# Performance work log

Measured on AMD Instinct MI355X. Metric: run time of the kernel, lower is better.

The kernel has to match this reference:

```python
import jax, jax.numpy as jnp
import numpy as np

# Quantization configuration mirroring the module-level constants in the source
INPUT_BIT, WEIGHT_BIT, OUTPUT_BIT, DAC_BIT, ADC_BIT = 8, 4, 8, 2, 8
N_SLICES = INPUT_BIT // DAC_BIT  # 4 bit-serial DAC slices of 2 bits each


def ste_round(v):
    # straight-through estimator round (fake-quant / LSQ style)
    return v + jax.lax.stop_gradient(jnp.round(v) - v)


def setup_inputs() -> dict:
    key = jax.random.key(0)
    k1, k2, k3 = jax.random.split(key, 3)
    B, IN_F, OUT_F = 32768, 1024, 1024
    x = jax.random.normal(k1, (B, IN_F), jnp.float32)
    weight = jax.random.normal(k2, (OUT_F, IN_F), jnp.float32) * 0.02
    bias = jax.random.normal(k3, (OUT_F,), jnp.float32) * 0.01
    # LSQ step sizes (learned scalars) for input / weight / output fake-quant
    s_x = jnp.float32(4.0 / 255.0)
    s_w = jnp.float32(0.01)
    s_o = jnp.float32(0.05)
    # per-output-column ADC gain (adc_adjust_mode='gain'); noise scales are 0 -> deterministic
    gain = jnp.ones((OUT_F,), jnp.float32)
    return {"x": x, "weight": weight, "bias": bias, "s_x": s_x, "s_w": s_w, "s_o": s_o, "gain": gain}


def reference(x, weight, bias, s_x, s_w, s_o, gain):
    QP_IN = float(2 ** INPUT_BIT - 1)                      # unsigned 8-bit activations
    QN_W, QP_W = float(-2 ** (WEIGHT_BIT - 1)), float(2 ** (WEIGHT_BIT - 1) - 1)  # signed 4-bit weights
    QN_A, QP_A = float(-2 ** (ADC_BIT - 1)), float(2 ** (ADC_BIT - 1) - 1)        # 8-bit ADC
    QN_O, QP_O = float(-2 ** (OUTPUT_BIT - 1)), float(2 ** (OUTPUT_BIT - 1) - 1)  # signed 8-bit output

    # --- input / weight fake quantization (LSQ) ---
    x_int = ste_round(jnp.clip(x / s_x, 0.0, QP_IN))       # [B, in_f] integer codes (float dtype)
    w_int = ste_round(jnp.clip(weight / s_w, QN_W, QP_W))  # [out_f, in_f]

    # ideal integer matmul result (differentiable path)
    ideal = jnp.matmul(x_int, w_int.T) * (s_x * s_w)       # [B, out_f]

    # --- bit-serial DAC slicing + per-slice ADC (hardware emulation, non-diff) ---
    xi = jax.lax.stop_gradient(x_int)
    wi = jax.lax.stop_gradient(w_int)
    g = jax.lax.stop_gradient(gain)                        # [out_f]
    base = float(2 ** DAC_BIT)
    acc = jnp.zeros((x.shape[0], weight.shape[0]), x.dtype)
    for i in range(N_SLICES):  # fixed small loop (4 slices)
        shift = base ** i
        sl = jnp.mod(jnp.floor(xi / shift), base)          # 2-bit slice in {0,1,2,3}
        partial = jnp.matmul(sl, wi.T)                     # analog MAC result [B, out_f]
        adc = jnp.clip(jnp.round(partial * g), QN_A, QP_A) / g  # ADC quant with column gain
        acc = acc + adc * shift
    out_cim = acc * (s_x * s_w)

    # straight-through: forward value = CIM-emulated, gradient = ideal path
    out = ideal + jax.lax.stop_gradient(out_cim - ideal) + bias

    # --- output fake quantization ---
    y = s_o * ste_round(jnp.clip(out / s_o, QN_O, QP_O))
    return y
```

## Files before the change

kernel.cpp:

```cpp
#pragma float_control(precise, on)
#include <hip/hip_runtime.h>
#include <stdint.h>


typedef int   i32x4 __attribute__((ext_vector_type(4)));

#define MDIM   32768
#define KDIM   1024
#define NDIM   1024
#define ABLK   131072

__device__ __forceinline__ void gload16(const void* g, void* l) {
  __builtin_amdgcn_global_load_lds(
      (const __attribute__((address_space(1))) void*)g,
      (__attribute__((address_space(3))) void*)l,
      16, 0, 0);
}

__global__ __launch_bounds__(256) void quant_x_kernel(
    const float* __restrict__ x, const float* __restrict__ s_x_p,
    uint8_t* __restrict__ Aq, uint8_t* __restrict__ rowFlag) {
  const float rcp = 1.0f / s_x_p[0];
  const int tid = blockIdx.x * 256 + threadIdx.x;
  const int m   = tid >> 6;
  const int k16 = tid & 63;
  const float* xp = x + (size_t)m * KDIM + k16 * 16;
  float vv[16];
#pragma unroll
  for (int q = 0; q < 4; ++q) {
    const float4 v = *(const float4*)(xp + q * 4);
    vv[q * 4 + 0] = v.x; vv[q * 4 + 1] = v.y; vv[q * 4 + 2] = v.z; vv[q * 4 + 3] = v.w;
  }
  int c[16];
  bool anyAmb = false;
#pragma unroll
  for (int j = 0; j < 16; ++j) {
    const float t  = vv[j] * rcp;
    const float tc = fminf(fmaxf(t, 0.0f), 255.0f);
    const float kf = rintf(tc);
    c[j] = (int)kf;
    const float d = 0.5f - fabsf(tc - kf);
    anyAmb = anyAmb || (d < 4e-7f * (tc + 1.0f));
  }
  if (anyAmb) rowFlag[m] = 1;
  const int bm  = m >> 5;
  const int wr  = (m >> 4) & 1;
  const int mi  = (m >> 2) & 3;
  const int fr4 = (m & 3) * 4;
  const int kt  = k16 >> 2, fk = k16 & 3;
  uint8_t* base = Aq + (size_t)bm * ABLK + kt * 8192 + ((wr * 4 + mi) << 10)
                  + (fk * 16 + fr4) * 16;
#pragma unroll
  for (int s = 0; s < 4; ++s) {
    uint32_t w[4];
#pragma unroll
    for (int q = 0; q < 4; ++q) {
      w[q] =  (uint32_t)((c[q*4+0] >> (2*s)) & 3)
           | ((uint32_t)((c[q*4+1] >> (2*s)) & 3) << 8)
           | ((uint32_t)((c[q*4+2] >> (2*s)) & 3) << 16)
           | ((uint32_t)((c[q*4+3] >> (2*s)) & 3) << 24);
    }
    *(uint4*)(base + s * 16) = make_uint4(w[0], w[1], w[2], w[3]);
  }
}

__global__ __launch_bounds__(256) void quant_w_kernel(
    const float* __restrict__ wgt, const float* __restrict__ s_w_p,
    uint8_t* __restrict__ Bq, int* __restrict__ colInfo) {
  const float rcp = 1.0f / s_w_p[0];
  const int tid = blockIdx.x * 256 + threadIdx.x;
  const int n   = tid >> 6;
  const int k16 = tid & 63;
  const float* wp = wgt + (size_t)n * KDIM + k16 * 16;
  float vv[16];
#pragma unroll
  for (int q = 0; q < 4; ++q) {
    const float4 v = *(const float4*)(wp + q * 4);
    vv[q * 4 + 0] = v.x; vv[q * 4 + 1] = v.y; vv[q * 4 + 2] = v.z; vv[q * 4 + 3] = v.w;
  }
  uint32_t w[4];
#pragma unroll
  for (int q = 0; q < 4; ++q) w[q] = 0;
#pragma unroll
  for (int j = 0; j < 16; ++j) {
    const float t  = vv[j] * rcp;
    const float tc = fminf(fmaxf(t, -8.0f), 7.0f);
    const float kf = rintf(tc);
    const int   iv = (int)kf;
    const float fr = tc - kf;
    const float d  = 0.5f - fabsf(fr);
    if (d < 4e-7f * (fabsf(tc) + 1.0f)) {
      const int jj = k16 * 16 + j;
      colInfo[n] = (jj << 2) | ((fr > 0.0f) ? 2 : 0) | 1;
    }
    w[j >> 2] |= (uint32_t)((uint8_t)iv) << (8 * (j & 3));
  }
  const int bn  = n >> 7;
  const int rl  = n & 127;
  const int wc  = rl >> 6;
  const int ni  = (rl >> 4) & 3;
  const int fr_ = rl & 15;
  const int kt  = k16 >> 2, fk = k16 & 3;
  uint8_t* dst = Bq + (size_t)bn * ABLK + kt * 8192 + ((wc * 4 + ni) << 10)
                 + (fk * 16 + fr_) * 16;
  *(uint4*)dst = make_uint4(w[0], w[1], w[2], w[3]);
}

struct ChainOut { float kf; float tc; };
__device__ __forceinline__ ChainOut cim_chain(float p0, float p1, float p2, float p3,
                                              float bi, float sxsw, float rcp_so) {
#pragma clang fp contract(off)
  const float a0 = fminf(fmaxf(p0, -128.f), 127.f);
  const float a1 = fminf(fmaxf(p1, -128.f), 127.f);
  const float a2 = fminf(fmaxf(p2, -128.f), 127.f);
  const float a3 = fminf(fmaxf(p3, -128.f), 127.f);
  float acc_i = a0 + a1 * 4.f;
  acc_i = acc_i + a2 * 16.f;
  acc_i = acc_i + a3 * 64.f;
  float idl_i = p0 + p1 * 4.f;
  idl_i = idl_i + p2 * 16.f;
  idl_i = idl_i + p3 * 64.f;
  const float cim  = acc_i * sxsw;
  const float idea = idl_i * sxsw;
  float ov = idea + (cim - idea);
  ov = ov + bi;
  const float t  = ov * rcp_so;
  const float tc = fminf(fmaxf(t, -128.f), 127.f);
  ChainOut r; r.kf = rintf(tc); r.tc = tc; return r;
}

__global__ __launch_bounds__(256) void gemm_cim(
    const uint8_t* __restrict__ Aq, const uint8_t* __restrict__ Bq,
    const float* __restrict__ bias, const float* __restrict__ gain,
    const float* __restrict__ s_x_p, const float* __restrict__ s_w_p,
    const float* __restrict__ s_o_p, const uint8_t* __restrict__ rowFlag,
    const int* __restrict__ colInfo, float* __restrict__ C) {
  __shared__ uint8_t sA[8192];
  __shared__ uint8_t sB[8192];

  const int t    = threadIdx.x;
  const int l    = (blockIdx.x & 7) * 1024 + (blockIdx.x >> 3);
  const int bn   = l & 7;
  const int bm   = l >> 3;
  const int lane = t & 63;
  const int wv   = t >> 6;
  const int wr   = wv >> 1, wc = wv & 1;
  const int fr   = lane & 15, lk = lane >> 4;

  const uint8_t* gA = Aq + (size_t)bm * ABLK;
  const uint8_t* gB = Bq + (size_t)bn * ABLK;

  i32x4 acc[4][4];
#pragma unroll
  for (int i = 0; i < 4; ++i)
#pragma unroll
    for (int j = 0; j < 4; ++j) acc[i][j] = (i32x4){0, 0, 0, 0};

  const int lofs = lane * 16;
  for (int kt = 0; kt < KDIM / 64; ++kt) {
    __syncthreads();
#pragma unroll
    for (int r = 0; r < 2; ++r) {
      const int o = t * 16 + r * 4096;
      gload16(gA + kt * 8192 + o, sA + o);
      gload16(gB + kt * 8192 + o, sB + o);
    }
    __syncthreads();

    i32x4 a[4], b[4];
#pragma unroll
    for (int mi = 0; mi < 4; ++mi)
      a[mi] = *(const i32x4*)(sA + ((wr * 4 + mi) << 10) + lofs);
#pragma unroll
    for (int ni = 0; ni < 4; ++ni)
      b[ni] = *(const i32x4*)(sB + ((wc * 4 + ni) << 10) + lofs);

#pragma unroll
    for (int mi = 0; mi < 4; ++mi)
#pragma unroll
      for (int ni = 0; ni < 4; ++ni)
        acc[mi][ni] = __builtin_amdgcn_mfma_i32_16x16x64_i8(a[mi], b[ni], acc[mi][ni], 0, 0, 0);
  }

  {
#pragma clang fp contract(off)
    const float sxf = s_x_p[0], swf = s_w_p[0], sof = s_o_p[0];
    const float sxsw   = sxf * swf;
    const float rcp_so = 1.0f / sof;
#pragma unroll
    for (int ni = 0; ni < 4; ++ni) {
      const int   col = bn * 128 + wc * 64 + ni * 16 + fr;
      const float g   = gain[col];
      const float bi  = bias[col];
      const int   ci  = colInfo[col];
#pragma unroll
      for (int mi = 0; mi < 4; ++mi) {
        const int rowA = bm * 128 + wr * 64 + mi * 16 + lk * 4;
        const int m    = rowA >> 2;
        const i32x4 pi = acc[mi][ni];
        const float p0 = (float)pi[0], p1 = (float)pi[1];
        const float p2 = (float)pi[2], p3 = (float)pi[3];
        float y;
        if (g == 1.0f) {
          const ChainOut c0 = cim_chain(p0, p1, p2, p3, bi, sxsw, rcp_so);
          bool done = false;
          if (ci & 1) {
            const int   jj  = ci >> 2;
            const float dir = (ci & 2) ? 1.f : -1.f;
            const uint8_t* ab = Aq + (size_t)(m >> 5) * ABLK + (jj >> 6) * 8192
                                + ((((m >> 4) & 1) * 4 + ((m >> 2) & 3)) << 10)
                                + ((((jj >> 4) & 3) * 16 + (m & 3) * 4) * 16) + (jj & 15);
            const float q0 = (float)ab[0];
            const float q1 = (float)ab[16];
            const float q2 = (float)ab[32];
            const float q3 = (float)ab[48];
            const ChainOut c1 = cim_chain(p0 + dir * q0, p1 + dir * q1,
                                          p2 + dir * q2, p3 + dir * q3,
                                          bi, sxsw, rcp_so);
            if (c1.kf != c0.kf) {
              y = sof * (0.5f * (c0.kf + c1.kf));
              done = true;
            }
          }
          if (!done) {
            const float frac = c0.tc - c0.kf;
            const float d    = 0.5f - fabsf(frac);
            const float eps  = rowFlag[m] ? 0.03f : 1e-3f;
            if (d < eps && frac != 0.0f)
              y = sof * (c0.kf + ((frac > 0.0f) ? 0.5f : -0.5f));
            else
              y = sof * c0.kf;
          }
        } else {
          float a0 = fminf(fmaxf(rintf(p0 * g), -128.f), 127.f) / g;
          float a1 = fminf(fmaxf(rintf(p1 * g), -128.f), 127.f) / g;
          float a2 = fminf(fmaxf(rintf(p2 * g), -128.f), 127.f) / g;
          float a3 = fminf(fmaxf(rintf(p3 * g), -128.f), 127.f) / g;
          float acc_i = ((a0 + a1 * 4.f) + a2 * 16.f) + a3 * 64.f;
          float idl_i = ((p0 + p1 * 4.f) + p2 * 16.f) + p3 * 64.f;
          float ov = idl_i * sxsw + (acc_i * sxsw - idl_i * sxsw) + bi;
          float tc = fminf(fmaxf(ov * rcp_so, -128.f), 127.f);
          y = sof * rintf(tc);
        }
        C[(size_t)m * NDIM + col] = y;
      }
    }
  }
}

extern "C" void kernel_launch(void* const* d_in, const int* in_sizes, int n_in,
                              void* d_out, int out_size, void* d_ws, size_t ws_size,
                              hipStream_t stream) {
  const float* x    = (const float*)d_in[0];
  const float* wgt  = (const float*)d_in[1];
  const float* bias = (const float*)d_in[2];
  const float* s_x  = (const float*)d_in[3];
  const float* s_w  = (const float*)d_in[4];
  const float* s_o  = (const float*)d_in[5];
  const float* gain = (const float*)d_in[6];
  float* C = (float*)d_out;

  const size_t aq_bytes = (size_t)1024 * ABLK;
  const size_t bq_bytes = (size_t)8 * ABLK;
  const size_t fl_bytes = MDIM + NDIM * sizeof(int);
  if (ws_size < aq_bytes + bq_bytes + fl_bytes) return;

  uint8_t* Aq      = (uint8_t*)d_ws;
  uint8_t* Bq      = Aq + aq_bytes;
  uint8_t* rowFlag = Bq + bq_bytes;
  int*     colInfo = (int*)(rowFlag + MDIM);

  hipMemsetAsync(rowFlag, 0, fl_bytes, stream);
  quant_x_kernel<<<dim3(8192), dim3(256), 0, stream>>>(x, s_x, Aq, rowFlag);
  quant_w_kernel<<<dim3(256),  dim3(256), 0, stream>>>(wgt, s_w, Bq, colInfo);
  gemm_cim<<<dim3(8192), dim3(256), 0, stream>>>(Aq, Bq, bias, gain, s_x, s_w, s_o,
                                                 rowFlag, colInfo, C);
}
```

Baseline: 285.5 us.

## Double-buffer LDS tiles in CIM GEMM to overlap global loads with MFMA

Splits the LDS staging buffers into two halves and prefetches the next K tile with direct global-to-LDS loads while the current tile is consumed by MFMA instructions. Partial vmcnt waits and raw s_barrier calls replace the two full __syncthreads per iteration. The goal is to hide global memory latency behind the int8 matrix work, at the cost of doubled LDS use (32 KB per block), which may lower occupancy. Correctness relies on the hand-written waitcnt counts and on LDS reads finishing before the buffer is overwritten.

```diff
diff --git a/kernel.cpp b/kernel.cpp
--- a/kernel.cpp
+++ b/kernel.cpp
@@ -135,8 +135,8 @@
     const float* __restrict__ s_x_p, const float* __restrict__ s_w_p,
     const float* __restrict__ s_o_p, const uint8_t* __restrict__ rowFlag,
     const int* __restrict__ colInfo, float* __restrict__ C) {
-  __shared__ uint8_t sA[8192];
-  __shared__ uint8_t sB[8192];
+  __shared__ uint8_t sA[2][8192];
+  __shared__ uint8_t sB[2][8192];
 
   const int t    = threadIdx.x;
   const int l    = (blockIdx.x & 7) * 1024 + (blockIdx.x >> 3);
@@ -157,30 +157,45 @@
     for (int j = 0; j < 4; ++j) acc[i][j] = (i32x4){0, 0, 0, 0};
 
   const int lofs = lane * 16;
-  for (int kt = 0; kt < KDIM / 64; ++kt) {
-    __syncthreads();
-#pragma unroll
-    for (int r = 0; r < 2; ++r) {
-      const int o = t * 16 + r * 4096;
-      gload16(gA + kt * 8192 + o, sA + o);
-      gload16(gB + kt * 8192 + o, sB + o);
-    }
-    __syncthreads();
-
+  const int o0 = t * 16, o1 = t * 16 + 4096;
+
+  auto STAGE = [&](int kt, int bf) {
+    gload16(gA + kt * 8192 + o0, sA[bf] + o0);
+    gload16(gA + kt * 8192 + o1, sA[bf] + o1);
+    gload16(gB + kt * 8192 + o0, sB[bf] + o0);
+    gload16(gB + kt * 8192 + o1, sB[bf] + o1);
+  };
+  auto COMPUTE = [&](int bf) {
     i32x4 a[4], b[4];
 #pragma unroll
     for (int mi = 0; mi < 4; ++mi)
-      a[mi] = *(const i32x4*)(sA + ((wr * 4 + mi) << 10) + lofs);
+      a[mi] = *(const i32x4*)(sA[bf] + ((wr * 4 + mi) << 10) + lofs);
 #pragma unroll
     for (int ni = 0; ni < 4; ++ni)
-      b[ni] = *(const i32x4*)(sB + ((wc * 4 + ni) << 10) + lofs);
-
+      b[ni] = *(const i32x4*)(sB[bf] + ((wc * 4 + ni) << 10) + lofs);
 #pragma unroll
     for (int mi = 0; mi < 4; ++mi)
 #pragma unroll
       for (int ni = 0; ni < 4; ++ni)
         acc[mi][ni] = __builtin_amdgcn_mfma_i32_16x16x64_i8(a[mi], b[ni], acc[mi][ni], 0, 0, 0);
-  }
+  };
+
+  STAGE(0, 0);
+  int cur = 0;
+  for (int kt = 0; kt < 15; ++kt) {
+    STAGE(kt + 1, cur ^ 1);
+    asm volatile("s_waitcnt vmcnt(4)" ::: "memory");
+    __builtin_amdgcn_sched_barrier(0);
+    __builtin_amdgcn_s_barrier();
+    COMPUTE(cur);
+    __builtin_amdgcn_sched_barrier(0);
+    __builtin_amdgcn_s_barrier();
+    cur ^= 1;
+  }
+  asm volatile("s_waitcnt vmcnt(0)" ::: "memory");
+  __builtin_amdgcn_sched_barrier(0);
+  __builtin_amdgcn_s_barrier();
+  COMPUTE(cur);
 
   {
 #pragma clang fp contract(off)
```

Measured after the change: 266.4 us. -6.7%, faster.

## Enlarge GEMM tile to 256x256 with 512 threads and triple-buffered LDS prefetch

Applied to the files above, without the earlier changes.

Doubles the GEMM block tile (256 rows of packed slices by 256 columns) and uses 8 waves per block. The quantized A/B packing is rearranged to match the new tile, and each wave now holds 8x4 accumulators. A three-stage LDS ring buffer issues global-to-LDS loads two k-steps ahead, interleaved with the MFMA bursts under explicit waitcnt, barriers and setprio. The goal is to raise data reuse and hide global load latency. In exchange it uses 96KB of LDS and more accumulator registers, which may limit occupancy, and adds many barriers per k-step.

```diff
diff --git a/kernel.cpp b/kernel.cpp
--- a/kernel.cpp
+++ b/kernel.cpp
@@ -3,12 +3,13 @@
 #include <stdint.h>
 
 
-typedef int   i32x4 __attribute__((ext_vector_type(4)));
+typedef int i32x4 __attribute__((ext_vector_type(4)));
 
 #define MDIM   32768
 #define KDIM   1024
 #define NDIM   1024
-#define ABLK   131072
+#define TBLK   262144
+#define KTS    16384
 
 __device__ __forceinline__ void gload16(const void* g, void* l) {
   __builtin_amdgcn_global_load_lds(
@@ -43,13 +44,11 @@
     anyAmb = anyAmb || (d < 4e-7f * (tc + 1.0f));
   }
   if (anyAmb) rowFlag[m] = 1;
-  const int bm  = m >> 5;
-  const int wr  = (m >> 4) & 1;
-  const int mi  = (m >> 2) & 3;
+  const int bm  = m >> 6;
+  const int g   = (m >> 2) & 15;
   const int fr4 = (m & 3) * 4;
-  const int kt  = k16 >> 2, fk = k16 & 3;
-  uint8_t* base = Aq + (size_t)bm * ABLK + kt * 8192 + ((wr * 4 + mi) << 10)
-                  + (fk * 16 + fr4) * 16;
+  const int kt  = k16 >> 2, kl = k16 & 3;
+  uint8_t* base = Aq + (size_t)bm * TBLK + kt * KTS + (g << 10) + (kl * 16 + fr4) * 16;
 #pragma unroll
   for (int s = 0; s < 4; ++s) {
     uint32_t w[4];
@@ -95,14 +94,12 @@
     }
     w[j >> 2] |= (uint32_t)((uint8_t)iv) << (8 * (j & 3));
   }
-  const int bn  = n >> 7;
-  const int rl  = n & 127;
-  const int wc  = rl >> 6;
-  const int ni  = (rl >> 4) & 3;
-  const int fr_ = rl & 15;
-  const int kt  = k16 >> 2, fk = k16 & 3;
-  uint8_t* dst = Bq + (size_t)bn * ABLK + kt * 8192 + ((wc * 4 + ni) << 10)
-                 + (fk * 16 + fr_) * 16;
+  const int bn  = n >> 8;
+  const int rr  = n & 255;
+  const int g   = rr >> 4;
+  const int fr_ = rr & 15;
+  const int kt  = k16 >> 2, kl = k16 & 3;
+  uint8_t* dst = Bq + (size_t)bn * TBLK + kt * KTS + (g << 10) + (kl * 16 + fr_) * 16;
   *(uint4*)dst = make_uint4(w[0], w[1], w[2], w[3]);
 }
 
@@ -129,57 +126,87 @@
   ChainOut r; r.kf = rintf(tc); r.tc = tc; return r;
 }
 
-__global__ __launch_bounds__(256) void gemm_cim(
+__global__ __launch_bounds__(512, 2) void gemm_cim(
     const uint8_t* __restrict__ Aq, const uint8_t* __restrict__ Bq,
     const float* __restrict__ bias, const float* __restrict__ gain,
     const float* __restrict__ s_x_p, const float* __restrict__ s_w_p,
     const float* __restrict__ s_o_p, const uint8_t* __restrict__ rowFlag,
     const int* __restrict__ colInfo, float* __restrict__ C) {
-  __shared__ uint8_t sA[8192];
-  __shared__ uint8_t sB[8192];
+  __shared__ uint8_t sA[3][16384];
+  __shared__ uint8_t sB[3][16384];
 
   const int t    = threadIdx.x;
-  const int l    = (blockIdx.x & 7) * 1024 + (blockIdx.x >> 3);
-  const int bn   = l & 7;
-  const int bm   = l >> 3;
+  const int l    = ((int)blockIdx.x & 7) * 256 + ((int)blockIdx.x >> 3);
+  const int bn   = l & 3;
+  const int bm   = l >> 2;
   const int lane = t & 63;
   const int wv   = t >> 6;
-  const int wr   = wv >> 1, wc = wv & 1;
+  const int wr   = wv >> 2, wc = wv & 3;
   const int fr   = lane & 15, lk = lane >> 4;
 
-  const uint8_t* gA = Aq + (size_t)bm * ABLK;
-  const uint8_t* gB = Bq + (size_t)bn * ABLK;
-
-  i32x4 acc[4][4];
-#pragma unroll
-  for (int i = 0; i < 4; ++i)
+  const uint8_t* gA = Aq + (size_t)bm * TBLK;
+  const uint8_t* gB = Bq + (size_t)bn * TBLK;
+
+  i32x4 acc[8][4];
+#pragma unroll
+  for (int i = 0; i < 8; ++i)
 #pragma unroll
     for (int j = 0; j < 4; ++j) acc[i][j] = (i32x4){0, 0, 0, 0};
 
   const int lofs = lane * 16;
-  for (int kt = 0; kt < KDIM / 64; ++kt) {
-    __syncthreads();
-#pragma unroll
-    for (int r = 0; r < 2; ++r) {
-      const int o = t * 16 + r * 4096;
-      gload16(gA + kt * 8192 + o, sA + o);
-      gload16(gB + kt * 8192 + o, sB + o);
+  const int o0 = t * 16, o1 = t * 16 + 8192;
+
+  auto STAGE_ALL = [&](int kt, int bf) {
+    gload16(gA + kt * KTS + o0, sA[bf] + o0);
+    gload16(gA + kt * KTS + o1, sA[bf] + o1);
+    gload16(gB + kt * KTS + o0, sB[bf] + o0);
+    gload16(gB + kt * KTS + o1, sB[bf] + o1);
+  };
+
+  STAGE_ALL(0, 0);
+  STAGE_ALL(1, 1);
+
+  for (int kt = 0; kt < 16; ++kt) {
+    const int bf = kt % 3;
+    const int pf = (kt + 2) % 3;
+    const bool doPf = (kt + 2) < 16;
+    if (kt < 15) asm volatile("s_waitcnt vmcnt(4)" ::: "memory");
+    else         asm volatile("s_waitcnt vmcnt(0)" ::: "memory");
+    __builtin_amdgcn_sched_barrier(0);
+    __builtin_amdgcn_s_barrier();
+
+    i32x4 b0, b1, b2, b3;
+#pragma unroll
+    for (int p = 0; p < 4; ++p) {
+      i32x4 a0 = *(const i32x4*)(sA[bf] + ((wr * 8 + 2 * p) << 10) + lofs);
+      i32x4 a1 = *(const i32x4*)(sA[bf] + ((wr * 8 + 2 * p + 1) << 10) + lofs);
+      if (p == 0) {
+        b0 = *(const i32x4*)(sB[bf] + ((wc * 4 + 0) << 10) + lofs);
+        b1 = *(const i32x4*)(sB[bf] + ((wc * 4 + 1) << 10) + lofs);
+        b2 = *(const i32x4*)(sB[bf] + ((wc * 4 + 2) << 10) + lofs);
+        b3 = *(const i32x4*)(sB[bf] + ((wc * 4 + 3) << 10) + lofs);
+      }
+      if (doPf) {
+        if      (p == 0) gload16(gA + (kt + 2) * KTS + o0, sA[pf] + o0);
+        else if (p == 1) gload16(gA + (kt + 2) * KTS + o1, sA[pf] + o1);
+        else if (p == 2) gload16(gB + (kt + 2) * KTS + o0, sB[pf] + o0);
+        else             gload16(gB + (kt + 2) * KTS + o1, sB[pf] + o1);
+      }
+      __builtin_amdgcn_s_barrier();
+      asm volatile("s_waitcnt lgkmcnt(0)" ::: "memory");
+      __builtin_amdgcn_sched_barrier(0);
+      __builtin_amdgcn_s_setprio(1);
+      acc[2*p  ][0] = __builtin_amdgcn_mfma_i32_16x16x64_i8(a0, b0, acc[2*p  ][0], 0, 0, 0);
+      acc[2*p  ][1] = __builtin_amdgcn_mfma_i32_16x16x64_i8(a0, b1, acc[2*p  ][1], 0, 0, 0);
+      acc[2*p  ][2] = __builtin_amdgcn_mfma_i32_16x16x64_i8(a0, b2, acc[2*p  ][2], 0, 0, 0);
+      acc[2*p  ][3] = __builtin_amdgcn_mfma_i32_16x16x64_i8(a0, b3, acc[2*p  ][3], 0, 0, 0);
+      acc[2*p+1][0] = __builtin_amdgcn_mfma_i32_16x16x64_i8(a1, b0, acc[2*p+1][0], 0, 0, 0);
+      acc[2*p+1][1] = __builtin_amdgcn_mfma_i32_16x16x64_i8(a1, b1, acc[2*p+1][1], 0, 0, 0);
+      acc[2*p+1][2] = __builtin_amdgcn_mfma_i32_16x16x64_i8(a1, b2, acc[2*p+1][2], 0, 0, 0);
+      acc[2*p+1][3] = __builtin_amdgcn_mfma_i32_16x16x64_i8(a1, b3, acc[2*p+1][3], 0, 0, 0);
+      __builtin_amdgcn_s_setprio(0);
+      __builtin_amdgcn_s_barrier();
     }
-    __syncthreads();
-
-    i32x4 a[4], b[4];
-#pragma unroll
-    for (int mi = 0; mi < 4; ++mi)
-      a[mi] = *(const i32x4*)(sA + ((wr * 4 + mi) << 10) + lofs);
-#pragma unroll
-    for (int ni = 0; ni < 4; ++ni)
-      b[ni] = *(const i32x4*)(sB + ((wc * 4 + ni) << 10) + lofs);
-
-#pragma unroll
-    for (int mi = 0; mi < 4; ++mi)
-#pragma unroll
-      for (int ni = 0; ni < 4; ++ni)
-        acc[mi][ni] = __builtin_amdgcn_mfma_i32_16x16x64_i8(a[mi], b[ni], acc[mi][ni], 0, 0, 0);
   }
 
   {
@@ -189,13 +216,13 @@
     const float rcp_so = 1.0f / sof;
 #pragma unroll
     for (int ni = 0; ni < 4; ++ni) {
-      const int   col = bn * 128 + wc * 64 + ni * 16 + fr;
+      const int   col = bn * 256 + wc * 64 + ni * 16 + fr;
       const float g   = gain[col];
       const float bi  = bias[col];
       const int   ci  = colInfo[col];
 #pragma unroll
-      for (int mi = 0; mi < 4; ++mi) {
-        const int rowA = bm * 128 + wr * 64 + mi * 16 + lk * 4;
+      for (int mi = 0; mi < 8; ++mi) {
+        const int rowA = bm * 256 + wr * 128 + mi * 16 + lk * 4;
         const int m    = rowA >> 2;
         const i32x4 pi = acc[mi][ni];
         const float p0 = (float)pi[0], p1 = (float)pi[1];
@@ -207,8 +234,8 @@
           if (ci & 1) {
             const int   jj  = ci >> 2;
             const float dir = (ci & 2) ? 1.f : -1.f;
-            const uint8_t* ab = Aq + (size_t)(m >> 5) * ABLK + (jj >> 6) * 8192
-                                + ((((m >> 4) & 1) * 4 + ((m >> 2) & 3)) << 10)
+            const uint8_t* ab = Aq + (size_t)(m >> 6) * TBLK + (jj >> 6) * KTS
+                                + (((m >> 2) & 15) << 10)
                                 + ((((jj >> 4) & 3) * 16 + (m & 3) * 4) * 16) + (jj & 15);
             const float q0 = (float)ab[0];
             const float q1 = (float)ab[16];
@@ -260,8 +287,8 @@
   const float* gain = (const float*)d_in[6];
   float* C = (float*)d_out;
 
-  const size_t aq_bytes = (size_t)1024 * ABLK;
-  const size_t bq_bytes = (size_t)8 * ABLK;
+  const size_t aq_bytes = (size_t)512 * TBLK;
+  const size_t bq_bytes = (size_t)4 * TBLK;
   const size_t fl_bytes = MDIM + NDIM * sizeof(int);
   if (ws_size < aq_bytes + bq_bytes + fl_bytes) return;
 
@@ -273,6 +300,6 @@
   hipMemsetAsync(rowFlag, 0, fl_bytes, stream);
   quant_x_kernel<<<dim3(8192), dim3(256), 0, stream>>>(x, s_x, Aq, rowFlag);
   quant_w_kernel<<<dim3(256),  dim3(256), 0, stream>>>(wgt, s_w, Bq, colInfo);
-  gemm_cim<<<dim3(8192), dim3(256), 0, stream>>>(Aq, Bq, bias, gain, s_x, s_w, s_o,
+  gemm_cim<<<dim3(2048), dim3(512), 0, stream>>>(Aq, Bq, bias, gain, s_x, s_w, s_o,
                                                  rowFlag, colInfo, C);
 }
```

Result: slower. 338.2 us (+18.5%).
